# Optimization experiments

Hardware: AMD Instinct MI355X
Metric: run time of the kernel (lower is better)

## Reference

```python
import jax, jax.numpy as jnp
import numpy as np

NUM_EMBEDDINGS = 1024
EMBEDDING_DIM = 256
SPLIT = 8
SPLIT_DIM = EMBEDDING_DIM // SPLIT  # 32
COMMITMENT_COST = 0.25
DECAY = 0.99
EPSILON = 1e-05


def setup_inputs() -> dict:
    key = jax.random.key(0)
    k1, k2, k3 = jax.random.split(key, 3)
    inputs = jax.random.normal(k1, (16384, EMBEDDING_DIM), dtype=jnp.float32)
    embedding = jax.random.normal(k2, (NUM_EMBEDDINGS, SPLIT_DIM), dtype=jnp.float32)
    ema_cluster_size = jnp.zeros((NUM_EMBEDDINGS,), dtype=jnp.float32)
    ema_w = jax.random.normal(k3, (NUM_EMBEDDINGS, SPLIT_DIM), dtype=jnp.float32)
    return {"inputs": inputs, "embedding": embedding,
            "ema_cluster_size": ema_cluster_size, "ema_w": ema_w}


def reference(inputs, embedding, ema_cluster_size, ema_w):
    B = inputs.shape[0]
    flat = inputs.reshape(-1, SPLIT_DIM)  # [B*split, d]
    rows = flat.shape[0]

    # squared euclidean distances to codebook: [rows, K]
    distances = (jnp.sum(flat ** 2, axis=1, keepdims=True)
                 + jnp.sum(embedding ** 2, axis=1)
                 - 2.0 * flat @ embedding.T)
    idx = jnp.argmin(distances, axis=1)  # [rows]

    # one-hot @ embedding == gather (same math, efficient form)
    quantized_flat = embedding[idx]  # [rows, d]

    # EMA statistics (training-mode update); quantization uses the OLD weights,
    # exactly as in the torch forward.
    counts = jax.ops.segment_sum(jnp.ones((rows,), jnp.float32), idx,
                                 num_segments=NUM_EMBEDDINGS)
    dw = jax.ops.segment_sum(flat, idx, num_segments=NUM_EMBEDDINGS)  # enc.T @ flat
    new_cs = ema_cluster_size * DECAY + (1.0 - DECAY) * counts
    n = jnp.sum(new_cs)
    new_cs = (new_cs + EPSILON) / (n + NUM_EMBEDDINGS * EPSILON) * n
    new_ema_w = ema_w * DECAY + (1.0 - DECAY) * dw
    new_embedding = new_ema_w / new_cs[:, None]

    # losses (EMA variant: only commitment term)
    e_latent_loss = jnp.mean((jax.lax.stop_gradient(quantized_flat) - flat) ** 2)
    loss = COMMITMENT_COST * e_latent_loss

    # straight-through estimator
    quantized_flat = flat + jax.lax.stop_gradient(quantized_flat - flat)
    quantized = quantized_flat.reshape(B, -1)  # [B, EMBEDDING_DIM]

    avg_probs = counts / rows  # mean of one-hot encodings over rows
    perplexity = jnp.exp(-jnp.sum(avg_probs * jnp.log(avg_probs + 1e-10)))

    encoding_indices = idx.reshape(B, SPLIT)
    return (loss, quantized, perplexity, encoding_indices,
            new_embedding, new_cs, new_ema_w)
```

## Files before the change

kernel.cpp:

```cpp
#include <hip/hip_runtime.h>

#define NUM_CODES 1024
#define DIM 32
#define ROWS 131072
#define DECAYF 0.99f
#define EPSF 1e-5f
#define CCOST 0.25f
#define SLAB 33792
#define RGROUPS 8
#define IBLK (SLAB / 256)
#define TILES_PER_CHUNK 16
#define DBIAS 256.0f

typedef __attribute__((ext_vector_type(8))) short short8v;
typedef __attribute__((ext_vector_type(4))) float f32x4;

__device__ __forceinline__ unsigned short bf16_rne(float f) {
    unsigned u = __float_as_uint(f);
    unsigned r = u + 0x7FFFu + ((u >> 16) & 1u);
    return (unsigned short)(r >> 16);
}

__global__ __launch_bounds__(256) void k_prep(const float* __restrict__ emb,
                                              unsigned short* __restrict__ bhi,
                                              unsigned short* __restrict__ blo,
                                              float* __restrict__ nbias,
                                              float* __restrict__ sumf2) {
    int s = blockIdx.x * 256 + threadIdx.x;
    if (s == 0) sumf2[0] = 0.0f;
    if (s < NUM_CODES) {
        const float4* e4 = (const float4*)(emb + s * DIM);
        float sum = 0.0f;
#pragma unroll
        for (int j = 0; j < 8; ++j) {
            float4 e = e4[j];
            sum += e.x * e.x + e.y * e.y + e.z * e.z + e.w * e.w;
        }
        nbias[s] = -0.5f * sum - DBIAS;
    }
    int l = s & 63, t = s >> 6;
    int code = t * 16 + (l & 15);
    int koff = (l >> 4) * 8;
    const float* src = emb + code * DIM + koff;
    float4 f0 = *(const float4*)(src);
    float4 f1 = *(const float4*)(src + 4);
    float fv[8] = {f0.x, f0.y, f0.z, f0.w, f1.x, f1.y, f1.z, f1.w};
    short8v h, lo;
#pragma unroll
    for (int j = 0; j < 8; ++j) {
        unsigned short hb = bf16_rne(fv[j]);
        float hf = __uint_as_float((unsigned)hb << 16);
        h[j]  = (short)hb;
        lo[j] = (short)bf16_rne(fv[j] - hf);
    }
    *(short8v*)(bhi + (size_t)s * 8) = h;
    *(short8v*)(blo + (size_t)s * 8) = lo;
}

__global__ __launch_bounds__(1024) void k_argmin(const float* __restrict__ flat,
                                                 const unsigned short* __restrict__ bhi_g,
                                                 const unsigned short* __restrict__ blo_g,
                                                 const float* __restrict__ nbias,
                                                 const float* __restrict__ emb,
                                                 int* __restrict__ idx_out,
                                                 float* __restrict__ idxf_out,
                                                 float* __restrict__ qout) {
    __shared__ short8v s_bh[4096];
    __shared__ short8v s_bl[4096];
    __shared__ float   s_nb[NUM_CODES];
    __shared__ unsigned s_win[4][256];
    __shared__ int     s_kwin[256];

    const int tid  = threadIdx.x;
    const int lane = tid & 63;
    const int wave = tid >> 6;
    const int c    = wave & 3;
    const int wrg  = wave >> 2;
    const int blockbase = blockIdx.x * 256;
    const int rowbase   = blockbase + wrg * 64;
    const int lr = lane & 15;
    const int lg = lane >> 4;

    {
        const short8v* gh = (const short8v*)bhi_g;
        const short8v* gl = (const short8v*)blo_g;
#pragma unroll
        for (int i = 0; i < 4; ++i) {
            s_bh[i * 1024 + tid] = gh[i * 1024 + tid];
            s_bl[i * 1024 + tid] = gl[i * 1024 + tid];
        }
        if (tid < NUM_CODES) s_nb[tid] = nbias[tid];
    }

    short8v ahi[4], alo[4];
#pragma unroll
    for (int rf = 0; rf < 4; ++rf) {
        const float* src = flat + (size_t)(rowbase + rf * 16 + lr) * DIM + lg * 8;
        float4 f0 = *(const float4*)src;
        float4 f1 = *(const float4*)(src + 4);
        float fv[8] = {f0.x, f0.y, f0.z, f0.w, f1.x, f1.y, f1.z, f1.w};
        short8v h, lo;
#pragma unroll
        for (int j = 0; j < 8; ++j) {
            unsigned short hb = bf16_rne(fv[j]);
            float hf = __uint_as_float((unsigned)hb << 16);
            h[j]  = (short)hb;
            lo[j] = (short)bf16_rne(fv[j] - hf);
        }
        ahi[rf] = h; alo[rf] = lo;
    }

    unsigned best[4][4];
#pragma unroll
    for (int rf = 0; rf < 4; ++rf)
#pragma unroll
        for (int q = 0; q < 4; ++q) best[rf][q] = 0xFFFFFFFFu;

    __syncthreads();

    const int t0 = c * TILES_PER_CHUNK;
#pragma unroll 2
    for (int tt = 0; tt < TILES_PER_CHUNK; ++tt) {
        const int t = t0 + tt;
        short8v bh = s_bh[t * 64 + lane];
        short8v bl = s_bl[t * 64 + lane];
        float nn   = s_nb[t * 16 + lr];
        unsigned code = (unsigned)(t * 16 + lr);
#pragma unroll
        for (int rf = 0; rf < 4; ++rf) {
            f32x4 acc = {nn, nn, nn, nn};
            acc = __builtin_amdgcn_mfma_f32_16x16x32_bf16(ahi[rf], bh, acc, 0, 0, 0);
            acc = __builtin_amdgcn_mfma_f32_16x16x32_bf16(ahi[rf], bl, acc, 0, 0, 0);
            acc = __builtin_amdgcn_mfma_f32_16x16x32_bf16(alo[rf], bh, acc, 0, 0, 0);
#pragma unroll
            for (int q = 0; q < 4; ++q) {
                unsigned pb = (__float_as_uint(acc[q]) & 0xFFFFFC00u) | code;
                best[rf][q] = min(best[rf][q], pb);
            }
        }
    }

#pragma unroll
    for (int rf = 0; rf < 4; ++rf) {
#pragma unroll
        for (int q = 0; q < 4; ++q) {
            unsigned b = best[rf][q];
#pragma unroll
            for (int m = 1; m < 16; m <<= 1)
                b = min(b, (unsigned)__shfl_xor((int)b, m));
            if (lr == q) s_win[c][wrg * 64 + rf * 16 + lg * 4 + q] = b;
        }
    }
    __syncthreads();

    if (tid < 256) {
        unsigned pm = min(min(s_win[0][tid], s_win[1][tid]),
                          min(s_win[2][tid], s_win[3][tid]));
        int k = (int)(pm & 1023u);
        s_kwin[tid] = k;
        idx_out[blockbase + tid]  = k;
        idxf_out[blockbase + tid] = (float)k;
    }
    __syncthreads();

#pragma unroll
    for (int h = 0; h < 2; ++h) {
        int i2  = h * 1024 + tid;
        int row = i2 >> 3, seg = i2 & 7;
        int k = s_kwin[row];
        float4 e = *(const float4*)(emb + (size_t)k * DIM + seg * 4);
        *(float4*)(qout + (size_t)(blockbase + row) * DIM + seg * 4) = e;
    }
}

__global__ __launch_bounds__(512) void k_scatter(const float* __restrict__ flat,
                                                 const int* __restrict__ idx,
                                                 float* __restrict__ slabs,
                                                 float* __restrict__ sumf2,
                                                 int rows_per_block) {
    __shared__ float acc[SLAB];
    __shared__ float red[512];
    const int tid = threadIdx.x;
    for (int i = tid; i < SLAB; i += 512) acc[i] = 0.0f;
    __syncthreads();

    const int row0 = blockIdx.x * rows_per_block;
    float sf = 0.0f;
    for (int rr = 0; rr < rows_per_block; rr += 512) {
        int r = row0 + rr + tid;
        int k = idx[r];
        const float4* f4 = (const float4*)(flat + (size_t)r * DIM);
        int kb = k * DIM;
#pragma unroll
        for (int j4 = 0; j4 < 8; ++j4) {
            float4 f = f4[j4];
            sf += f.x * f.x + f.y * f.y + f.z * f.z + f.w * f.w;
            int j = 4 * j4;
            atomicAdd(&acc[kb + ((j + 0 + k) & 31)], f.x);
            atomicAdd(&acc[kb + ((j + 1 + k) & 31)], f.y);
            atomicAdd(&acc[kb + ((j + 2 + k) & 31)], f.z);
            atomicAdd(&acc[kb + ((j + 3 + k) & 31)], f.w);
        }
        atomicAdd(&acc[32768 + k], 1.0f);
    }
    __syncthreads();

    float* slab = slabs + (size_t)blockIdx.x * SLAB;
    for (int i = tid; i < 32768; i += 512) {
        int k = i >> 5, j = i & 31;
        slab[i] = acc[(i & ~31) | ((j + k) & 31)];
    }
    for (int i = tid; i < NUM_CODES; i += 512) slab[32768 + i] = acc[32768 + i];

    red[tid] = sf;
    __syncthreads();
    for (int s = 256; s > 0; s >>= 1) {
        if (tid < s) red[tid] += red[tid + s];
        __syncthreads();
    }
    if (tid == 0) atomicAdd(sumf2, red[0]);
}

__global__ __launch_bounds__(256) void k_reduce1(const float* __restrict__ slabs,
                                                 float* __restrict__ partial,
                                                 int pcount) {
    int g  = blockIdx.x / IBLK;
    int ib = blockIdx.x % IBLK;
    int i = ib * 256 + threadIdx.x;
    const float* base = slabs + (size_t)g * pcount * SLAB + i;
    float s = 0.0f;
#pragma unroll 4
    for (int p = 0; p < pcount; ++p) s += base[(size_t)p * SLAB];
    partial[(size_t)g * SLAB + i] = s;
}

__global__ __launch_bounds__(256) void k_reduce2(const float* __restrict__ partial,
                                                 float* __restrict__ dw_sum,
                                                 float* __restrict__ counts_sum) {
    int i = blockIdx.x * 256 + threadIdx.x;
    float s = 0.0f;
#pragma unroll
    for (int g = 0; g < RGROUPS; ++g) s += partial[(size_t)g * SLAB + i];
    if (i < 32768) dw_sum[i] = s;
    else           counts_sum[i - 32768] = s;
}

__global__ __launch_bounds__(1024) void k_final(const float* __restrict__ ema_cs,
                                                const float* __restrict__ ema_w,
                                                const float* __restrict__ emb,
                                                const float* __restrict__ counts,
                                                const float* __restrict__ dw,
                                                const float* __restrict__ sumf2,
                                                float* __restrict__ out_loss,
                                                float* __restrict__ out_perp,
                                                float* __restrict__ out_emb,
                                                float* __restrict__ out_cs,
                                                float* __restrict__ out_ema_w) {
    int tid = threadIdx.x;
    __shared__ float s_cs[NUM_CODES];
    __shared__ float s_cnt[NUM_CODES];
    __shared__ float red[1024];
    __shared__ double redd[1024];

    float c = counts[tid];
    s_cnt[tid] = c;
    float pre = ema_cs[tid] * DECAYF + (1.0f - DECAYF) * c;

    red[tid] = pre;
    __syncthreads();
    for (int s = 512; s > 0; s >>= 1) {
        if (tid < s) red[tid] += red[tid + s];
        __syncthreads();
    }
    float n = red[0];
    __syncthreads();

    float ncs = (pre + EPSF) / (n + (float)NUM_CODES * EPSF) * n;
    s_cs[tid] = ncs;
    out_cs[tid] = ncs;

    float p = c / (float)ROWS;
    red[tid] = p * logf(p + 1e-10f);
    __syncthreads();
    for (int s = 512; s > 0; s >>= 1) {
        if (tid < s) red[tid] += red[tid + s];
        __syncthreads();
    }
    float nplogp = red[0];
    __syncthreads();

    double lterm = 0.0;
    for (int i = tid; i < NUM_CODES * DIM; i += 1024) {
        int k = i >> 5;
        float dwv = dw[i];
        float e = emb[i];
        lterm += (double)e * ((double)e * (double)s_cnt[k] - 2.0 * (double)dwv);
        float w = ema_w[i] * DECAYF + (1.0f - DECAYF) * dwv;
        out_ema_w[i] = w;
        out_emb[i] = w / s_cs[k];
    }
    redd[tid] = lterm;
    __syncthreads();
    for (int s = 512; s > 0; s >>= 1) {
        if (tid < s) redd[tid] += redd[tid + s];
        __syncthreads();
    }
    if (tid == 0) {
        double lsum = (double)sumf2[0] + redd[0];
        out_loss[0] = (float)(CCOST * lsum / (double)((size_t)ROWS * DIM));
        out_perp[0] = expf(-nplogp);
    }
}

extern "C" void kernel_launch(void* const* d_in, const int* in_sizes, int n_in,
                              void* d_out, int out_size, void* d_ws, size_t ws_size,
                              hipStream_t stream) {
    const float* inputs    = (const float*)d_in[0];
    const float* embedding = (const float*)d_in[1];
    const float* ema_cs    = (const float*)d_in[2];
    const float* ema_w     = (const float*)d_in[3];

    float* out        = (float*)d_out;
    float* out_loss   = out;
    float* out_q      = out + 1;
    float* out_perp   = out + 4194305;
    float* out_idxf   = out + 4194306;
    float* out_emb    = out + 4325378;
    float* out_cs     = out + 4358146;
    float* out_ema_w  = out + 4359170;

    char* ws = (char*)d_ws;
    float* nbias      = (float*)(ws);
    float* sumf2      = (float*)(ws + 4096);
    int*   idx        = (int*)(ws + 8192);
    unsigned short* bhi_g = (unsigned short*)(ws + 532480);
    unsigned short* blo_g = (unsigned short*)(ws + 598016);
    float* dw_sum     = (float*)(ws + 663552);
    float* counts_sum = (float*)(ws + 794624);
    float* partial    = (float*)(ws + 798720);
    float* slabs      = (float*)(ws + 1880064);

    size_t slab_off = 1880064;
    size_t avail = (ws_size > slab_off) ? (ws_size - slab_off) : 0;
    int P = 32;
    if (avail >= (size_t)256 * SLAB * 4) P = 256;
    else if (avail >= (size_t)128 * SLAB * 4) P = 128;
    else if (avail >= (size_t)64 * SLAB * 4) P = 64;
    int rows_per_block = ROWS / P;

    k_prep   <<<16, 256, 0, stream>>>(embedding, bhi_g, blo_g, nbias, sumf2);
    k_argmin <<<ROWS / 256, 1024, 0, stream>>>(inputs, bhi_g, blo_g, nbias, embedding,
                                               idx, out_idxf, out_q);
    k_scatter<<<P, 512, 0, stream>>>(inputs, idx, slabs, sumf2, rows_per_block);
    k_reduce1<<<RGROUPS * IBLK, 256, 0, stream>>>(slabs, partial, P / RGROUPS);
    k_reduce2<<<IBLK, 256, 0, stream>>>(partial, dw_sum, counts_sum);
    k_final  <<<1, 1024, 0, stream>>>(ema_cs, ema_w, embedding, counts_sum, dw_sum,
                                      sumf2, out_loss, out_perp, out_emb, out_cs,
                                      out_ema_w);
}
```

Baseline: 104.3 us.

## Process two row tiles per argmin block and merge slab reduction into one kernel

The argmin kernel now covers 512 rows per block in two sequential passes, so each block's shared-memory load of the split bf16 codebook is reused for twice as many rows and half as many blocks are launched. The two-level slab reduction becomes a single kernel that sums all P slabs per element, removing one launch and the intermediate partial buffer. The default minimum P rises to 64. The trade-offs are fewer argmin blocks, which is less latency hiding, and longer serial per-thread loops in a reduction with few blocks.

```diff
diff --git a/kernel.cpp b/kernel.cpp
--- a/kernel.cpp
+++ b/kernel.cpp
@@ -7,9 +7,9 @@
 #define EPSF 1e-5f
 #define CCOST 0.25f
 #define SLAB 33792
-#define RGROUPS 8
 #define IBLK (SLAB / 256)
 #define TILES_PER_CHUNK 16
+#define ROWS_PER_ABLOCK 512
 #define DBIAS 256.0f
 
 typedef __attribute__((ext_vector_type(8))) short short8v;
@@ -68,18 +68,18 @@
     __shared__ short8v s_bh[4096];
     __shared__ short8v s_bl[4096];
     __shared__ float   s_nb[NUM_CODES];
-    __shared__ unsigned s_win[4][256];
-    __shared__ int     s_kwin[256];
+    __shared__ unsigned s_win[4][ROWS_PER_ABLOCK];
+    __shared__ int     s_kwin[ROWS_PER_ABLOCK];
 
     const int tid  = threadIdx.x;
     const int lane = tid & 63;
     const int wave = tid >> 6;
     const int c    = wave & 3;
     const int wrg  = wave >> 2;
-    const int blockbase = blockIdx.x * 256;
-    const int rowbase   = blockbase + wrg * 64;
+    const int blockbase = blockIdx.x * ROWS_PER_ABLOCK;
     const int lr = lane & 15;
     const int lg = lane >> 4;
+    const int t0 = c * TILES_PER_CHUNK;
 
     {
         const short8v* gh = (const short8v*)bhi_g;
@@ -91,69 +91,73 @@
         }
         if (tid < NUM_CODES) s_nb[tid] = nbias[tid];
     }
-
-    short8v ahi[4], alo[4];
-#pragma unroll
-    for (int rf = 0; rf < 4; ++rf) {
-        const float* src = flat + (size_t)(rowbase + rf * 16 + lr) * DIM + lg * 8;
-        float4 f0 = *(const float4*)src;
-        float4 f1 = *(const float4*)(src + 4);
-        float fv[8] = {f0.x, f0.y, f0.z, f0.w, f1.x, f1.y, f1.z, f1.w};
-        short8v h, lo;
-#pragma unroll
-        for (int j = 0; j < 8; ++j) {
-            unsigned short hb = bf16_rne(fv[j]);
-            float hf = __uint_as_float((unsigned)hb << 16);
-            h[j]  = (short)hb;
-            lo[j] = (short)bf16_rne(fv[j] - hf);
-        }
-        ahi[rf] = h; alo[rf] = lo;
-    }
-
-    unsigned best[4][4];
-#pragma unroll
-    for (int rf = 0; rf < 4; ++rf)
-#pragma unroll
-        for (int q = 0; q < 4; ++q) best[rf][q] = 0xFFFFFFFFu;
-
-    __syncthreads();
-
-    const int t0 = c * TILES_PER_CHUNK;
+    __syncthreads();
+
+#pragma unroll 1
+    for (int pass = 0; pass < 2; ++pass) {
+        const int rowbase = blockbase + pass * 256 + wrg * 64;
+
+        short8v ahi[4], alo[4];
+#pragma unroll
+        for (int rf = 0; rf < 4; ++rf) {
+            const float* src = flat + (size_t)(rowbase + rf * 16 + lr) * DIM + lg * 8;
+            float4 f0 = *(const float4*)src;
+            float4 f1 = *(const float4*)(src + 4);
+            float fv[8] = {f0.x, f0.y, f0.z, f0.w, f1.x, f1.y, f1.z, f1.w};
+            short8v h, lo;
+#pragma unroll
+            for (int j = 0; j < 8; ++j) {
+                unsigned short hb = bf16_rne(fv[j]);
+                float hf = __uint_as_float((unsigned)hb << 16);
+                h[j]  = (short)hb;
+                lo[j] = (short)bf16_rne(fv[j] - hf);
+            }
+            ahi[rf] = h; alo[rf] = lo;
+        }
+
+        unsigned best[4][4];
+#pragma unroll
+        for (int rf = 0; rf < 4; ++rf)
+#pragma unroll
+            for (int q = 0; q < 4; ++q) best[rf][q] = 0xFFFFFFFFu;
+
 #pragma unroll 2
-    for (int tt = 0; tt < TILES_PER_CHUNK; ++tt) {
-        const int t = t0 + tt;
-        short8v bh = s_bh[t * 64 + lane];
-        short8v bl = s_bl[t * 64 + lane];
-        float nn   = s_nb[t * 16 + lr];
-        unsigned code = (unsigned)(t * 16 + lr);
+        for (int tt = 0; tt < TILES_PER_CHUNK; ++tt) {
+            const int t = t0 + tt;
+            short8v bh = s_bh[t * 64 + lane];
+            short8v bl = s_bl[t * 64 + lane];
+            float nn   = s_nb[t * 16 + lr];
+            unsigned code = (unsigned)(t * 16 + lr);
+#pragma unroll
+            for (int rf = 0; rf < 4; ++rf) {
+                f32x4 acc = {nn, nn, nn, nn};
+                acc = __builtin_amdgcn_mfma_f32_16x16x32_bf16(ahi[rf], bh, acc, 0, 0, 0);
+                acc = __builtin_amdgcn_mfma_f32_16x16x32_bf16(ahi[rf], bl, acc, 0, 0, 0);
+                acc = __builtin_amdgcn_mfma_f32_16x16x32_bf16(alo[rf], bh, acc, 0, 0, 0);
+#pragma unroll
+                for (int q = 0; q < 4; ++q) {
+                    unsigned pb = (__float_as_uint(acc[q]) & 0xFFFFFC00u) | code;
+                    best[rf][q] = min(best[rf][q], pb);
+                }
+            }
+        }
+
 #pragma unroll
         for (int rf = 0; rf < 4; ++rf) {
-            f32x4 acc = {nn, nn, nn, nn};
-            acc = __builtin_amdgcn_mfma_f32_16x16x32_bf16(ahi[rf], bh, acc, 0, 0, 0);
-            acc = __builtin_amdgcn_mfma_f32_16x16x32_bf16(ahi[rf], bl, acc, 0, 0, 0);
-            acc = __builtin_amdgcn_mfma_f32_16x16x32_bf16(alo[rf], bh, acc, 0, 0, 0);
 #pragma unroll
             for (int q = 0; q < 4; ++q) {
-                unsigned pb = (__float_as_uint(acc[q]) & 0xFFFFFC00u) | code;
-                best[rf][q] = min(best[rf][q], pb);
+                unsigned b = best[rf][q];
+#pragma unroll
+                for (int m = 1; m < 16; m <<= 1)
+                    b = min(b, (unsigned)__shfl_xor((int)b, m));
+                if (lr == q)
+                    s_win[c][pass * 256 + wrg * 64 + rf * 16 + lg * 4 + q] = b;
             }
         }
     }
-
-#pragma unroll
-    for (int rf = 0; rf < 4; ++rf) {
-#pragma unroll
-        for (int q = 0; q < 4; ++q) {
-            unsigned b = best[rf][q];
-#pragma unroll
-            for (int m = 1; m < 16; m <<= 1)
-                b = min(b, (unsigned)__shfl_xor((int)b, m));
-            if (lr == q) s_win[c][wrg * 64 + rf * 16 + lg * 4 + q] = b;
-        }
-    }
-    __syncthreads();
-
-    if (tid < 256) {
+    __syncthreads();
+
+    if (tid < ROWS_PER_ABLOCK) {
         unsigned pm = min(min(s_win[0][tid], s_win[1][tid]),
                           min(s_win[2][tid], s_win[3][tid]));
         int k = (int)(pm & 1023u);
@@ -164,7 +168,7 @@
     __syncthreads();
 
 #pragma unroll
-    for (int h = 0; h < 2; ++h) {
+    for (int h = 0; h < 4; ++h) {
         int i2  = h * 1024 + tid;
         int row = i2 >> 3, seg = i2 & 7;
         int k = s_kwin[row];
@@ -221,26 +225,14 @@
     if (tid == 0) atomicAdd(sumf2, red[0]);
 }
 
-__global__ __launch_bounds__(256) void k_reduce1(const float* __restrict__ slabs,
-                                                 float* __restrict__ partial,
-                                                 int pcount) {
-    int g  = blockIdx.x / IBLK;
-    int ib = blockIdx.x % IBLK;
-    int i = ib * 256 + threadIdx.x;
-    const float* base = slabs + (size_t)g * pcount * SLAB + i;
+__global__ __launch_bounds__(256) void k_reduce(const float* __restrict__ slabs,
+                                                float* __restrict__ dw_sum,
+                                                float* __restrict__ counts_sum,
+                                                int P) {
+    int i = blockIdx.x * 256 + threadIdx.x;
     float s = 0.0f;
 #pragma unroll 4
-    for (int p = 0; p < pcount; ++p) s += base[(size_t)p * SLAB];
-    partial[(size_t)g * SLAB + i] = s;
-}
-
-__global__ __launch_bounds__(256) void k_reduce2(const float* __restrict__ partial,
-                                                 float* __restrict__ dw_sum,
-                                                 float* __restrict__ counts_sum) {
-    int i = blockIdx.x * 256 + threadIdx.x;
-    float s = 0.0f;
-#pragma unroll
-    for (int g = 0; g < RGROUPS; ++g) s += partial[(size_t)g * SLAB + i];
+    for (int p = 0; p < P; ++p) s += slabs[(size_t)p * SLAB + i];
     if (i < 32768) dw_sum[i] = s;
     else           counts_sum[i - 32768] = s;
 }
@@ -337,23 +329,21 @@
     unsigned short* blo_g = (unsigned short*)(ws + 598016);
     float* dw_sum     = (float*)(ws + 663552);
     float* counts_sum = (float*)(ws + 794624);
-    float* partial    = (float*)(ws + 798720);
-    float* slabs      = (float*)(ws + 1880064);
-
-    size_t slab_off = 1880064;
+    float* slabs      = (float*)(ws + 798720);
+
+    size_t slab_off = 798720;
     size_t avail = (ws_size > slab_off) ? (ws_size - slab_off) : 0;
-    int P = 32;
+    int P = 64;
     if (avail >= (size_t)256 * SLAB * 4) P = 256;
     else if (avail >= (size_t)128 * SLAB * 4) P = 128;
-    else if (avail >= (size_t)64 * SLAB * 4) P = 64;
     int rows_per_block = ROWS / P;
 
     k_prep   <<<16, 256, 0, stream>>>(embedding, bhi_g, blo_g, nbias, sumf2);
-    k_argmin <<<ROWS / 256, 1024, 0, stream>>>(inputs, bhi_g, blo_g, nbias, embedding,
-                                               idx, out_idxf, out_q);
+    k_argmin <<<ROWS / ROWS_PER_ABLOCK, 1024, 0, stream>>>(inputs, bhi_g, blo_g,
+                                                           nbias, embedding,
+                                                           idx, out_idxf, out_q);
     k_scatter<<<P, 512, 0, stream>>>(inputs, idx, slabs, sumf2, rows_per_block);
-    k_reduce1<<<RGROUPS * IBLK, 256, 0, stream>>>(slabs, partial, P / RGROUPS);
-    k_reduce2<<<IBLK, 256, 0, stream>>>(partial, dw_sum, counts_sum);
+    k_reduce <<<IBLK, 256, 0, stream>>>(slabs, dw_sum, counts_sum, P);
     k_final  <<<1, 1024, 0, stream>>>(ema_cs, ema_w, embedding, counts_sum, dw_sum,
                                       sumf2, out_loss, out_perp, out_emb, out_cs,
                                       out_ema_w);
```

After: 114.8 us. +10.0%, slower.
